# Kernel optimization log

Hardware: AMD Instinct MI355X
Metric: run time of the kernel (lower is better)

## Reference

```python
import jax, jax.numpy as jnp
import numpy as np

N_NODES = 100000
N_EDGES = 1600000
HIDDEN = 128
EF_DIM = 16
LAYERS = 2
N_GRAPHS = 64


def _residual(x, W, b):
    # Residual(mlp_num=2): x + act(act(x@W0+b0)@W1+b1), act = silu
    h = jax.nn.silu(x @ W[0] + b[0])
    h = jax.nn.silu(h @ W[1] + b[1])
    return x + h


def setup_inputs() -> dict:
    key = jax.random.key(0)
    ks = jax.random.split(key, 10)
    scalar = jax.random.normal(ks[0], (N_NODES, HIDDEN), jnp.float32)
    ef = jax.random.normal(ks[1], (N_EDGES, EF_DIM), jnp.float32)
    edge_index = jax.random.randint(ks[2], (2, N_EDGES), 0, N_NODES, jnp.int32)
    C = jax.random.uniform(ks[3], (N_NODES, 1), dtype=jnp.float32)
    conv_smooth = jax.random.uniform(ks[4], (N_EDGES, 1), dtype=jnp.float32)
    batch_index = jnp.sort(jax.random.randint(ks[5], (N_NODES,), 0, N_GRAPHS, jnp.int32))
    # per VD_Conv layer: emb0, emb1, conv0, conv1, out0, out1 residual blocks; + 3 pooling blocks
    n_res = LAYERS * 6 + 3
    res_W = jax.random.normal(ks[6], (n_res, 2, HIDDEN, HIDDEN), jnp.float32) * 0.02
    res_b = jnp.zeros((n_res, 2, HIDDEN), jnp.float32)
    e_lin = jax.random.normal(ks[7], (LAYERS, EF_DIM, HIDDEN), jnp.float32) * 0.02
    return {"scalar": scalar, "ef": ef, "edge_index": edge_index, "C": C,
            "conv_smooth": conv_smooth, "batch_index": batch_index,
            "res_W": res_W, "res_b": res_b, "e_lin": e_lin}


def reference(scalar, ef, edge_index, C, conv_smooth, batch_index, res_W, res_b, e_lin):
    row, col = edge_index[0], edge_index[1]
    for i in range(LAYERS):
        p = 6 * i
        s_src = _residual(scalar, res_W[p], res_b[p])
        s_dst = _residual(scalar, res_W[p + 1], res_b[p + 1])
        conv_filter = (ef @ e_lin[i]) * conv_smooth            # [E, H]
        scalar_edge = s_dst[col] * conv_filter                 # gather + elementwise filter
        conv = jax.ops.segment_sum(scalar_edge, row, num_segments=N_NODES) * C  # scatter-reduce (agg='sum')
        conv = _residual(_residual(conv, res_W[p + 2], res_b[p + 2]), res_W[p + 3], res_b[p + 3])
        s = s_src * conv
        s = _residual(_residual(s, res_W[p + 4], res_b[p + 4]), res_W[p + 5], res_b[p + 5])
        scalar = s + scalar                                    # outer residual in Vanilla_DisGNN
    graph = jax.ops.segment_sum(scalar, batch_index, num_segments=N_GRAPHS)
    q = 6 * LAYERS
    for j in range(3):
        graph = _residual(graph, res_W[q + j], res_b[q + j])
    return graph
```

## Files before the change

### kernel.cpp

```cpp
#include <hip/hip_runtime.h>
#include <hip/hip_bf16.h>
#include <cstdint>
#include <cstddef>

#define HD 128
#define WOFF 16384

typedef __bf16    bf16x8 __attribute__((ext_vector_type(8)));
typedef float     f32x4  __attribute__((ext_vector_type(4)));
typedef float     f32x16 __attribute__((ext_vector_type(16)));
typedef _Float16  h2     __attribute__((ext_vector_type(2)));
typedef _Float16  h8     __attribute__((ext_vector_type(8)));

typedef __attribute__((address_space(1))) const unsigned char ga_u8;
typedef __attribute__((address_space(3))) unsigned char lds_u8;

#if defined(__has_builtin)
#if __has_builtin(__builtin_amdgcn_fdot2)
#define HAVE_FDOT2 1
#endif
#endif

__device__ __forceinline__ float fdot2f(h2 a, h2 b, float c) {
#ifdef HAVE_FDOT2
    return __builtin_amdgcn_fdot2(a, b, c, false);
#else
    return c + (float)a[0]*(float)b[0] + (float)a[1]*(float)b[1];
#endif
}

__device__ __forceinline__ int swz(int r, int byteInRow) {
    int chunk = (byteInRow >> 4) ^ (r & 7);
    return r * 256 + (chunk << 4) + (byteInRow & 15);
}

__device__ __forceinline__ float silu_f(float v) { return v / (1.f + __expf(-v)); }

__device__ __forceinline__ int crow32(int r, int lane) {
    return (r & 3) + 8 * (r >> 2) + 4 * (lane >> 5);
}


__device__ __forceinline__ void issue_wstage(const __bf16* __restrict__ w, char* lds, int tid) {
    const int wv = tid >> 6, lane = tid & 63;
    const char* g = (const char*)w;
    #pragma unroll
    for (int i = 0; i < 4; ++i) {
        const int seg = (wv << 2) | i;
        __builtin_amdgcn_global_load_lds(
            (ga_u8*)(g + seg * 1024 + lane * 16),
            (lds_u8*)(lds + WOFF + seg * 1024),
            16, 0, 0);
    }
}

__device__ __forceinline__ void stage_x64(const float* __restrict__ x, char* lds,
                                          int r0, int nrows, int tid) {
    const int q = tid & 15;
    #pragma unroll
    for (int rr = 0; rr < 2; ++rr) {
        const int r  = (tid >> 4) + rr * 32;
        const int gr = r0 + r;
        float4 a = {0,0,0,0}, b = {0,0,0,0};
        if (gr < nrows) {
            const float4* p = (const float4*)(x + (size_t)gr * HD + q * 8);
            a = p[0]; b = p[1];
        }
        bf16x8 v;
        v[0]=(__bf16)a.x; v[1]=(__bf16)a.y; v[2]=(__bf16)a.z; v[3]=(__bf16)a.w;
        v[4]=(__bf16)b.x; v[5]=(__bf16)b.y; v[6]=(__bf16)b.z; v[7]=(__bf16)b.w;
        *(bf16x8*)(lds + swz(r, q * 16)) = v;
    }
}

__device__ __forceinline__ void mm_pass32(const char* lds, const float* __restrict__ bias,
                                          int rowtile, int coltile, int lane,
                                          f32x16& accA, f32x16& accB) {
    const int rowA = rowtile * 32 + (lane & 31);
    const int rowB = coltile * 32 + (lane & 31);
    const int kb   = (lane >> 5) * 16;
    bf16x8 afr[8];
    #pragma unroll
    for (int s = 0; s < 8; ++s)
        afr[s] = *(const bf16x8*)(lds + swz(rowA, s * 32 + kb));
    const float bv = bias[coltile * 32 + (lane & 31)];
    #pragma unroll
    for (int r = 0; r < 16; ++r) { accA[r] = bv; accB[r] = 0.f; }
    #pragma unroll
    for (int s = 0; s < 8; s += 2) {
        const bf16x8 b0 = *(const bf16x8*)(lds + WOFF + swz(rowB, s * 32 + kb));
        accA = __builtin_amdgcn_mfma_f32_32x32x16_bf16(afr[s], b0, accA, 0, 0, 0);
        const bf16x8 b1 = *(const bf16x8*)(lds + WOFF + swz(rowB, (s + 1) * 32 + kb));
        accB = __builtin_amdgcn_mfma_f32_32x32x16_bf16(afr[s + 1], b1, accB, 0, 0, 0);
    }
}

__device__ __forceinline__ void write_h32(char* lds, const f32x16& aA, const f32x16& aB,
                                          int rowtile, int coltile, int lane) {
    const int colb = (coltile * 32 + (lane & 31)) * 2;
    #pragma unroll
    for (int r = 0; r < 16; ++r)
        *(__bf16*)(lds + swz(rowtile * 32 + crow32(r, lane), colb)) =
            (__bf16)silu_f(aA[r] + aB[r]);
}

__device__ __forceinline__ void restage32(char* lds, const float carry[16],
                                          int rowtile, int coltile, int lane) {
    const int colb = (coltile * 32 + (lane & 31)) * 2;
    #pragma unroll
    for (int r = 0; r < 16; ++r)
        *(__bf16*)(lds + swz(rowtile * 32 + crow32(r, lane), colb)) = (__bf16)carry[r];
}

__global__ __launch_bounds__(512) void resid_dual_kernel(
    const float* __restrict__ x,
    const __bf16* __restrict__ wtA, const float* __restrict__ bA,
    const __bf16* __restrict__ wtB, const float* __restrict__ bB,
    __bf16* __restrict__ out1, __bf16* __restrict__ out2, int nrows)
{
    __shared__ char lds[49152];
    const int tid = threadIdx.x, lane = tid & 63, wv = tid >> 6;
    const int rowtile = wv >> 2, coltile = wv & 3;
    const int r0 = blockIdx.x * 64;
    const int colg = coltile * 32 + (lane & 31);

    issue_wstage(wtA, lds, tid);
    stage_x64(x, lds, r0, nrows, tid);
    f32x16 accA, accB;
    float xe[16];
    #pragma unroll
    for (int r = 0; r < 16; ++r) {
        const int gr = r0 + rowtile * 32 + crow32(r, lane);
        xe[r] = (gr < nrows) ? x[(size_t)gr * HD + colg] : 0.f;
    }
    __syncthreads();

    mm_pass32(lds, bA, rowtile, coltile, lane, accA, accB);
    __syncthreads();
    issue_wstage(wtA + 16384, lds, tid);
    write_h32(lds, accA, accB, rowtile, coltile, lane);
    __syncthreads();
    mm_pass32(lds, bA + HD, rowtile, coltile, lane, accA, accB);
    #pragma unroll
    for (int r = 0; r < 16; ++r) {
        const int gr = r0 + rowtile * 32 + crow32(r, lane);
        if (gr < nrows)
            out1[(size_t)gr * HD + colg] = (__bf16)(xe[r] + silu_f(accA[r] + accB[r]));
    }
    __syncthreads();
    issue_wstage(wtB, lds, tid);
    restage32(lds, xe, rowtile, coltile, lane);
    __syncthreads();
    mm_pass32(lds, bB, rowtile, coltile, lane, accA, accB);
    __syncthreads();
    issue_wstage(wtB + 16384, lds, tid);
    write_h32(lds, accA, accB, rowtile, coltile, lane);
    __syncthreads();
    mm_pass32(lds, bB + HD, rowtile, coltile, lane, accA, accB);
    #pragma unroll
    for (int r = 0; r < 16; ++r) {
        const int gr = r0 + rowtile * 32 + crow32(r, lane);
        if (gr < nrows)
            out2[(size_t)gr * HD + colg] = (__bf16)(xe[r] + silu_f(accA[r] + accB[r]));
    }
}

__global__ __launch_bounds__(512) void chain4_kernel(
    const float* __restrict__ x, const __bf16* __restrict__ mid,
    const __bf16* __restrict__ wA, const float* __restrict__ bA,
    const __bf16* __restrict__ wB, const float* __restrict__ bB,
    const __bf16* __restrict__ wC, const float* __restrict__ bC,
    const __bf16* __restrict__ wD, const float* __restrict__ bD,
    const float* __restrict__ post, float* __restrict__ y, int nrows)
{
    __shared__ char lds[49152];
    const int tid = threadIdx.x, lane = tid & 63, wv = tid >> 6;
    const int rowtile = wv >> 2, coltile = wv & 3;
    const int r0 = blockIdx.x * 64;
    const int colg = coltile * 32 + (lane & 31);

    issue_wstage(wA, lds, tid);
    stage_x64(x, lds, r0, nrows, tid);
    f32x16 accA, accB;
    float carry[16];
    #pragma unroll
    for (int r = 0; r < 16; ++r) {
        const int gr = r0 + rowtile * 32 + crow32(r, lane);
        carry[r] = (gr < nrows) ? x[(size_t)gr * HD + colg] : 0.f;
    }
    __syncthreads();

    mm_pass32(lds, bA, rowtile, coltile, lane, accA, accB);
    __syncthreads();
    issue_wstage(wA + 16384, lds, tid);
    write_h32(lds, accA, accB, rowtile, coltile, lane);
    __syncthreads();
    mm_pass32(lds, bA + HD, rowtile, coltile, lane, accA, accB);
    #pragma unroll
    for (int r = 0; r < 16; ++r) carry[r] += silu_f(accA[r] + accB[r]);
    __syncthreads();
    issue_wstage(wB, lds, tid);
    restage32(lds, carry, rowtile, coltile, lane);
    __syncthreads();
    mm_pass32(lds, bB, rowtile, coltile, lane, accA, accB);
    __syncthreads();
    issue_wstage(wB + 16384, lds, tid);
    write_h32(lds, accA, accB, rowtile, coltile, lane);
    __syncthreads();
    mm_pass32(lds, bB + HD, rowtile, coltile, lane, accA, accB);
    #pragma unroll
    for (int r = 0; r < 16; ++r) {
        const int gr = r0 + rowtile * 32 + crow32(r, lane);
        const float m = (gr < nrows) ? (float)mid[(size_t)gr * HD + colg] : 0.f;
        carry[r] = (carry[r] + silu_f(accA[r] + accB[r])) * m;
    }
    __syncthreads();
    issue_wstage(wC, lds, tid);
    restage32(lds, carry, rowtile, coltile, lane);
    __syncthreads();
    mm_pass32(lds, bC, rowtile, coltile, lane, accA, accB);
    __syncthreads();
    issue_wstage(wC + 16384, lds, tid);
    write_h32(lds, accA, accB, rowtile, coltile, lane);
    __syncthreads();
    mm_pass32(lds, bC + HD, rowtile, coltile, lane, accA, accB);
    #pragma unroll
    for (int r = 0; r < 16; ++r) carry[r] += silu_f(accA[r] + accB[r]);
    __syncthreads();
    issue_wstage(wD, lds, tid);
    restage32(lds, carry, rowtile, coltile, lane);
    __syncthreads();
    mm_pass32(lds, bD, rowtile, coltile, lane, accA, accB);
    __syncthreads();
    issue_wstage(wD + 16384, lds, tid);
    write_h32(lds, accA, accB, rowtile, coltile, lane);
    __syncthreads();
    mm_pass32(lds, bD + HD, rowtile, coltile, lane, accA, accB);
    #pragma unroll
    for (int r = 0; r < 16; ++r) {
        const int gr = r0 + rowtile * 32 + crow32(r, lane);
        if (gr < nrows)
            y[(size_t)gr * HD + colg] =
                carry[r] + silu_f(accA[r] + accB[r]) + post[(size_t)gr * HD + colg];
    }
}

__global__ __launch_bounds__(512) void chain3_kernel(
    const float* __restrict__ x,
    const __bf16* __restrict__ wA, const float* __restrict__ bA,
    const __bf16* __restrict__ wB, const float* __restrict__ bB,
    const __bf16* __restrict__ wC, const float* __restrict__ bC,
    float* __restrict__ y, int nrows)
{
    __shared__ char lds[49152];
    const int tid = threadIdx.x, lane = tid & 63, wv = tid >> 6;
    const int rowtile = wv >> 2, coltile = wv & 3;
    const int r0 = blockIdx.x * 64;
    const int colg = coltile * 32 + (lane & 31);

    issue_wstage(wA, lds, tid);
    stage_x64(x, lds, r0, nrows, tid);
    f32x16 accA, accB;
    float carry[16];
    #pragma unroll
    for (int r = 0; r < 16; ++r) {
        const int gr = r0 + rowtile * 32 + crow32(r, lane);
        carry[r] = (gr < nrows) ? x[(size_t)gr * HD + colg] : 0.f;
    }
    __syncthreads();

    const __bf16* w1s[3] = {wA + 16384, wB + 16384, wC + 16384};
    const __bf16* w0next[3] = {wB, wC, nullptr};
    const float* bs[3] = {bA, bB, bC};
    #pragma unroll
    for (int sb = 0; sb < 3; ++sb) {
        mm_pass32(lds, bs[sb], rowtile, coltile, lane, accA, accB);
        __syncthreads();
        issue_wstage(w1s[sb], lds, tid);
        write_h32(lds, accA, accB, rowtile, coltile, lane);
        __syncthreads();
        mm_pass32(lds, bs[sb] + HD, rowtile, coltile, lane, accA, accB);
        #pragma unroll
        for (int r = 0; r < 16; ++r) carry[r] += silu_f(accA[r] + accB[r]);
        if (sb < 2) {
            __syncthreads();
            issue_wstage(w0next[sb], lds, tid);
            restage32(lds, carry, rowtile, coltile, lane);
            __syncthreads();
        }
    }
    #pragma unroll
    for (int r = 0; r < 16; ++r) {
        const int gr = r0 + rowtile * 32 + crow32(r, lane);
        if (gr < nrows)
            y[(size_t)gr * HD + colg] = carry[r];
    }
}

__global__ __launch_bounds__(256) void hist_kernel(const int* __restrict__ erow, int* __restrict__ cnt, int E) {
    int i = blockIdx.x * blockDim.x + threadIdx.x;
    const int stride = gridDim.x * blockDim.x;
    for (; i < E; i += stride) atomicAdd(&cnt[erow[i]], 1);
}

__global__ __launch_bounds__(256) void scan1_kernel(const int* __restrict__ cnt, int* __restrict__ part, int n) {
    __shared__ int red[256];
    const int base = blockIdx.x * 1024;
    int s = 0;
    for (int i = threadIdx.x; i < 1024; i += 256) {
        const int idx = base + i;
        s += (idx < n) ? cnt[idx] : 0;
    }
    red[threadIdx.x] = s; __syncthreads();
    for (int o = 128; o > 0; o >>= 1) {
        if (threadIdx.x < o) red[threadIdx.x] += red[threadIdx.x + o];
        __syncthreads();
    }
    if (threadIdx.x == 0) part[blockIdx.x] = red[0];
}

__global__ __launch_bounds__(256) void scan2_kernel(int* __restrict__ part, int nb,
                                                    int* __restrict__ rowptr, int n) {
    __shared__ int sh[257];
    const int tid = threadIdx.x;
    int a[4]; int s = 0;
    #pragma unroll
    for (int q = 0; q < 4; ++q) {
        const int i = tid*4 + q;
        a[q] = (i < nb) ? part[i] : 0;
        s += a[q];
    }
    sh[tid + 1] = s; __syncthreads();
    if (tid == 0) {
        sh[0] = 0;
        int run = 0;
        for (int i = 1; i <= 256; ++i) { run += sh[i]; sh[i] = run; }
    }
    __syncthreads();
    int off = sh[tid];
    #pragma unroll
    for (int q = 0; q < 4; ++q) {
        const int i = tid*4 + q;
        if (i < nb) part[i] = off;
        off += a[q];
    }
    if (tid == 255) rowptr[n] = off;
}

__global__ __launch_bounds__(256) void scan3_kernel(const int* __restrict__ cnt, const int* __restrict__ part,
                                                    int* __restrict__ rowptr, int n) {
    __shared__ int sc[257];
    const int base = blockIdx.x * 1024;
    const int i0 = base + threadIdx.x * 4;
    int v[4]; int s = 0;
    #pragma unroll
    for (int q = 0; q < 4; ++q) {
        const int idx = i0 + q;
        v[q] = (idx < n) ? cnt[idx] : 0;
        s += v[q];
    }
    sc[threadIdx.x + 1] = s; __syncthreads();
    if (threadIdx.x == 0) {
        int run = 0;
        for (int i = 0; i < 256; ++i) { const int t = sc[i + 1]; sc[i + 1] = run; run += t; }
    }
    __syncthreads();
    int off = part[blockIdx.x] + sc[threadIdx.x + 1];
    #pragma unroll
    for (int q = 0; q < 4; ++q) {
        const int idx = i0 + q;
        if (idx < n) rowptr[idx] = off;
        off += v[q];
    }
}

__global__ __launch_bounds__(256) void scatter_reorder_kernel(
    const int* __restrict__ erow, const int* __restrict__ ecol,
    const float* __restrict__ ef, const float* __restrict__ cs,
    const int* __restrict__ rowptr, int* __restrict__ cursor,
    int* __restrict__ csr_col, _Float16* __restrict__ csr_ef, int E)
{
    int i = blockIdx.x * blockDim.x + threadIdx.x;
    const int stride = gridDim.x * blockDim.x;
    for (; i < E; i += stride) {
        const int r = erow[i];
        const int p = rowptr[r] + atomicAdd(&cursor[r], 1);
        csr_col[p] = ecol[i];
        const float c = cs[i];
        const float4* ep = (const float4*)(ef + (size_t)i * 16);
        const float4 e0 = ep[0], e1 = ep[1], e2 = ep[2], e3 = ep[3];
        h8 v0, v1;
        v0[0]=(_Float16)(e0.x*c); v0[1]=(_Float16)(e0.y*c); v0[2]=(_Float16)(e0.z*c); v0[3]=(_Float16)(e0.w*c);
        v0[4]=(_Float16)(e1.x*c); v0[5]=(_Float16)(e1.y*c); v0[6]=(_Float16)(e1.z*c); v0[7]=(_Float16)(e1.w*c);
        v1[0]=(_Float16)(e2.x*c); v1[1]=(_Float16)(e2.y*c); v1[2]=(_Float16)(e2.z*c); v1[3]=(_Float16)(e2.w*c);
        v1[4]=(_Float16)(e3.x*c); v1[5]=(_Float16)(e3.y*c); v1[6]=(_Float16)(e3.z*c); v1[7]=(_Float16)(e3.w*c);
        h8* dst = (h8*)(csr_ef + (size_t)p * 16);
        dst[0] = v0; dst[1] = v1;
    }
}

__global__ __launch_bounds__(256) void elin16_kernel(const float* __restrict__ elin,
                                                     _Float16* __restrict__ out, int total) {
    const int i = blockIdx.x * 256 + threadIdx.x;
    if (i < total) out[i] = (_Float16)elin[i];
}

__device__ __forceinline__ float bfu_lo(uint32_t u) { return __uint_as_float(u << 16); }
__device__ __forceinline__ float bfu_hi(uint32_t u) { return __uint_as_float(u & 0xffff0000u); }

__device__ __forceinline__ void edge_dot(const h8 a0, const h8 a1,
                                         const h2 w0[8], const h2 w1[8],
                                         float& f0, float& f1) {
    #pragma unroll
    for (int kk = 0; kk < 4; ++kk) {
        h2 p = {a0[2*kk], a0[2*kk+1]};
        f0 = fdot2f(p, w0[kk], f0);
        f1 = fdot2f(p, w1[kk], f1);
    }
    #pragma unroll
    for (int kk = 0; kk < 4; ++kk) {
        h2 p = {a1[2*kk], a1[2*kk+1]};
        f0 = fdot2f(p, w0[4+kk], f0);
        f1 = fdot2f(p, w1[4+kk], f1);
    }
}

__global__ __launch_bounds__(256) void conv_kernel(
    const _Float16* __restrict__ csr_ef, const int* __restrict__ csr_col,
    const _Float16* __restrict__ elin16, const int* __restrict__ rowptr,
    const __bf16* __restrict__ sdst, const float* __restrict__ Cn,
    float* __restrict__ conv, int nnodes)
{
    const int wv   = __builtin_amdgcn_readfirstlane(threadIdx.x >> 6);
    const int lane = threadIdx.x & 63;
    const int v = blockIdx.x * 4 + wv;
    if (v >= nnodes) return;
    const int j0 = lane * 2;

    h2 w0[8], w1[8];
    #pragma unroll
    for (int kk = 0; kk < 8; ++kk) {
        w0[kk][0] = elin16[(2*kk)   * HD + j0];
        w0[kk][1] = elin16[(2*kk+1) * HD + j0];
        w1[kk][0] = elin16[(2*kk)   * HD + j0 + 1];
        w1[kk][1] = elin16[(2*kk+1) * HD + j0 + 1];
    }

    const uint16_t* sd = (const uint16_t*)sdst;
    const int beg = rowptr[v], end = rowptr[v + 1];
    float acc0 = 0.f, acc1 = 0.f;
    int t = beg;
    for (; t + 8 <= end; t += 8) {
        int c[8];
        #pragma unroll
        for (int q = 0; q < 8; ++q) c[q] = csr_col[t + q];
        uint32_t u[8];
        #pragma unroll
        for (int q = 0; q < 8; ++q)
            u[q] = *(const uint32_t*)(sd + (size_t)c[q] * HD + j0);
        #pragma unroll
        for (int q = 0; q < 8; ++q) {
            const h8* ep = (const h8*)(csr_ef + (size_t)(t + q) * 16);
            const h8 a0 = ep[0], a1 = ep[1];
            float f0 = 0.f, f1 = 0.f;
            edge_dot(a0, a1, w0, w1, f0, f1);
            acc0 = fmaf(bfu_lo(u[q]), f0, acc0);
            acc1 = fmaf(bfu_hi(u[q]), f1, acc1);
        }
    }
    for (; t + 2 <= end; t += 2) {
        int c[2];
        c[0] = csr_col[t]; c[1] = csr_col[t + 1];
        uint32_t u[2];
        u[0] = *(const uint32_t*)(sd + (size_t)c[0] * HD + j0);
        u[1] = *(const uint32_t*)(sd + (size_t)c[1] * HD + j0);
        #pragma unroll
        for (int q = 0; q < 2; ++q) {
            const h8* ep = (const h8*)(csr_ef + (size_t)(t + q) * 16);
            const h8 a0 = ep[0], a1 = ep[1];
            float f0 = 0.f, f1 = 0.f;
            edge_dot(a0, a1, w0, w1, f0, f1);
            acc0 = fmaf(bfu_lo(u[q]), f0, acc0);
            acc1 = fmaf(bfu_hi(u[q]), f1, acc1);
        }
    }
    if (t < end) {
        const int c = csr_col[t];
        const uint32_t u = *(const uint32_t*)(sd + (size_t)c * HD + j0);
        const h8* ep = (const h8*)(csr_ef + (size_t)t * 16);
        const h8 a0 = ep[0], a1 = ep[1];
        float f0 = 0.f, f1 = 0.f;
        edge_dot(a0, a1, w0, w1, f0, f1);
        acc0 = fmaf(bfu_lo(u), f0, acc0);
        acc1 = fmaf(bfu_hi(u), f1, acc1);
    }
    const float cn = Cn[v];
    float2 out = {acc0 * cn, acc1 * cn};
    *(float2*)(conv + (size_t)v * HD + j0) = out;
}

__global__ __launch_bounds__(256) void pool_kernel(
    const float* __restrict__ s, const int* __restrict__ bidx,
    float* __restrict__ g, int n)
{
    const int slot = threadIdx.x >> 5;
    const int jc   = (threadIdx.x & 31) * 4;
    const int base = blockIdx.x * 256;
    if (base >= n) return;
    const int end = (base + 256 < n) ? base + 256 : n;
    float4 acc = {0,0,0,0};
    int cur = -1;
    for (int i = base + slot; i < end; i += 8) {
        const int b = bidx[i];
        if (b != cur) {
            if (cur >= 0) {
                atomicAdd(g + (size_t)cur*HD + jc + 0, acc.x);
                atomicAdd(g + (size_t)cur*HD + jc + 1, acc.y);
                atomicAdd(g + (size_t)cur*HD + jc + 2, acc.z);
                atomicAdd(g + (size_t)cur*HD + jc + 3, acc.w);
            }
            acc = {0,0,0,0};
            cur = b;
        }
        const float4 v = *(const float4*)(s + (size_t)i*HD + jc);
        acc.x += v.x; acc.y += v.y; acc.z += v.z; acc.w += v.w;
    }
    if (cur >= 0) {
        atomicAdd(g + (size_t)cur*HD + jc + 0, acc.x);
        atomicAdd(g + (size_t)cur*HD + jc + 1, acc.y);
        atomicAdd(g + (size_t)cur*HD + jc + 2, acc.z);
        atomicAdd(g + (size_t)cur*HD + jc + 3, acc.w);
    }
}

__global__ __launch_bounds__(256) void convw_kernel(const float* __restrict__ W, __bf16* __restrict__ wt, int total) {
    const int idx = blockIdx.x * 256 + threadIdx.x;
    if (idx >= total) return;
    const int mat = idx >> 14;
    const int rem = idx & 16383;
    const int j = rem >> 7;
    const int b = rem & 127;
    const int c = b >> 3, e = b & 7;
    const int k = ((c ^ (j & 7)) << 3) | e;
    wt[idx] = (__bf16)W[(size_t)mat * 16384 + k * HD + j];
}

extern "C" void kernel_launch(void* const* d_in, const int* in_sizes, int n_in,
                              void* d_out, int out_size, void* d_ws, size_t ws_size,
                              hipStream_t stream) {
    const float* scalar = (const float*)d_in[0];
    const float* ef     = (const float*)d_in[1];
    const int*   eidx   = (const int*)  d_in[2];
    const float* Cn     = (const float*)d_in[3];
    const float* cs     = (const float*)d_in[4];
    const int*   bidx   = (const int*)  d_in[5];
    const float* resW   = (const float*)d_in[6];
    const float* resB   = (const float*)d_in[7];
    const float* elin   = (const float*)d_in[8];

    const int N      = in_sizes[0] / HD;
    const int E      = in_sizes[1] / 16;
    const int n_res  = in_sizes[7] / (2 * HD);
    const int layers = (n_res - 3) / 6;
    const int G      = out_size / HD;
    const size_t nfeat = (size_t)N * HD;

    char* p = (char*)d_ws;
    auto alloc = [&](size_t bytes) { char* q = p; p += (bytes + 255) & ~(size_t)255; return q; };
    float*    A      = (float*)alloc(nfeat * 4);
    float*    Dc     = (float*)alloc(nfeat * 4);
    __bf16*   Bs16   = (__bf16*)alloc(nfeat * 2);
    __bf16*   Cs16   = (__bf16*)alloc(nfeat * 2);
    __bf16*   wt     = (__bf16*)alloc((size_t)n_res * 2 * 16384 * 2);
    float*    graph  = (float*)alloc((size_t)G * HD * 4);
    int*      rowptr = (int*)alloc((size_t)(N + 1) * 4);
    int*      rowcnt = (int*)alloc((size_t)N * 4);
    int*      csr_col= (int*)alloc((size_t)E * 4);
    _Float16* csr_ef = (_Float16*)alloc((size_t)E * 16 * 2);
    _Float16* elin16 = (_Float16*)alloc((size_t)layers * 16 * HD * 2);
    int*      part   = (int*)alloc(1024 * 4);

    const int* erow = eidx;
    const int* ecol = eidx + E;

    const int totW = n_res * 2 * 16384;
    convw_kernel<<<(totW + 255) / 256, 256, 0, stream>>>(resW, wt, totW);
    const int totE = layers * 16 * HD;
    elin16_kernel<<<(totE + 255) / 256, 256, 0, stream>>>(elin, elin16, totE);

    const int nchunks = (N + 1023) / 1024;
    hipMemsetAsync(rowcnt, 0, (size_t)N * 4, stream);
    hist_kernel<<<1024, 256, 0, stream>>>(erow, rowcnt, E);
    scan1_kernel<<<nchunks, 256, 0, stream>>>(rowcnt, part, N);
    scan2_kernel<<<1, 256, 0, stream>>>(part, nchunks, rowptr, N);
    scan3_kernel<<<nchunks, 256, 0, stream>>>(rowcnt, part, rowptr, N);
    hipMemsetAsync(rowcnt, 0, (size_t)N * 4, stream);
    scatter_reorder_kernel<<<1024, 256, 0, stream>>>(erow, ecol, ef, cs, rowptr, rowcnt, csr_col, csr_ef, E);

    const int gridR = (N + 63) / 64;
    const float* cur = scalar;
    for (int i = 0; i < layers; ++i) {
        const int pb = 6 * i;
        resid_dual_kernel<<<gridR, 512, 0, stream>>>(
            cur,
            wt + (size_t)pb * 32768, resB + (size_t)pb * 256,
            wt + (size_t)(pb + 1) * 32768, resB + (size_t)(pb + 1) * 256,
            Bs16, Cs16, N);
        conv_kernel<<<(N + 3) / 4, 256, 0, stream>>>(
            csr_ef, csr_col, elin16 + (size_t)i * 16 * HD, rowptr, Cs16, Cn, Dc, N);
        chain4_kernel<<<gridR, 512, 0, stream>>>(
            Dc, Bs16,
            wt + (size_t)(pb + 2) * 32768, resB + (size_t)(pb + 2) * 256,
            wt + (size_t)(pb + 3) * 32768, resB + (size_t)(pb + 3) * 256,
            wt + (size_t)(pb + 4) * 32768, resB + (size_t)(pb + 4) * 256,
            wt + (size_t)(pb + 5) * 32768, resB + (size_t)(pb + 5) * 256,
            cur, A, N);
        cur = A;
    }

    hipMemsetAsync(graph, 0, (size_t)G * HD * 4, stream);
    pool_kernel<<<(N + 255) / 256, 256, 0, stream>>>(cur, bidx, graph, N);

    const int q = 6 * layers;
    const int gridG = (G + 63) / 64;
    chain3_kernel<<<gridG, 512, 0, stream>>>(
        graph,
        wt + (size_t)q * 32768, resB + (size_t)q * 256,
        wt + (size_t)(q + 1) * 32768, resB + (size_t)(q + 1) * 256,
        wt + (size_t)(q + 2) * 32768, resB + (size_t)(q + 2) * 256,
        (float*)d_out, G);
}
```

Measured before the change: 876.0 us.

## Double-buffer weight staging in LDS and widen swizzle to 16 chunks

Adds a second LDS weight buffer to the fused residual-MLP kernels. The next weight matrix is now prefetched with global_load_lds while the current MFMA pass runs, instead of being loaded after a barrier, which hides weight-load latency behind compute. The LDS swizzle XOR pattern is widened from 8 to 16 chunks, matched in the weight pre-transform kernel, to cut bank conflicts. The cost is LDS use rising from 48KB to 80KB per block, which can lower the number of resident blocks per CU.

```diff
diff --git a/kernel.cpp b/kernel.cpp
--- a/kernel.cpp
+++ b/kernel.cpp
@@ -4,7 +4,9 @@
 #include <cstddef>
 
 #define HD 128
-#define WOFF 16384
+#define WB0 16384
+#define WB1 49152
+#define LDS_SZ 81920
 
 typedef __bf16    bf16x8 __attribute__((ext_vector_type(8)));
 typedef float     f32x4  __attribute__((ext_vector_type(4)));
@@ -30,7 +32,7 @@
 }
 
 __device__ __forceinline__ int swz(int r, int byteInRow) {
-    int chunk = (byteInRow >> 4) ^ (r & 7);
+    int chunk = (byteInRow >> 4) ^ (r & 15);
     return r * 256 + (chunk << 4) + (byteInRow & 15);
 }
 
@@ -41,7 +43,8 @@
 }
 
 
-__device__ __forceinline__ void issue_wstage(const __bf16* __restrict__ w, char* lds, int tid) {
+__device__ __forceinline__ void issue_wstage(const __bf16* __restrict__ w, char* lds,
+                                             int woff, int tid) {
     const int wv = tid >> 6, lane = tid & 63;
     const char* g = (const char*)w;
     #pragma unroll
@@ -49,7 +52,7 @@
         const int seg = (wv << 2) | i;
         __builtin_amdgcn_global_load_lds(
             (ga_u8*)(g + seg * 1024 + lane * 16),
-            (lds_u8*)(lds + WOFF + seg * 1024),
+            (lds_u8*)(lds + woff + seg * 1024),
             16, 0, 0);
     }
 }
@@ -73,7 +76,8 @@
     }
 }
 
-__device__ __forceinline__ void mm_pass32(const char* lds, const float* __restrict__ bias,
+__device__ __forceinline__ void mm_pass32(const char* lds, int woff,
+                                          const float* __restrict__ bias,
                                           int rowtile, int coltile, int lane,
                                           f32x16& accA, f32x16& accB) {
     const int rowA = rowtile * 32 + (lane & 31);
@@ -88,9 +92,9 @@
     for (int r = 0; r < 16; ++r) { accA[r] = bv; accB[r] = 0.f; }
     #pragma unroll
     for (int s = 0; s < 8; s += 2) {
-        const bf16x8 b0 = *(const bf16x8*)(lds + WOFF + swz(rowB, s * 32 + kb));
+        const bf16x8 b0 = *(const bf16x8*)(lds + woff + swz(rowB, s * 32 + kb));
         accA = __builtin_amdgcn_mfma_f32_32x32x16_bf16(afr[s], b0, accA, 0, 0, 0);
-        const bf16x8 b1 = *(const bf16x8*)(lds + WOFF + swz(rowB, (s + 1) * 32 + kb));
+        const bf16x8 b1 = *(const bf16x8*)(lds + woff + swz(rowB, (s + 1) * 32 + kb));
         accB = __builtin_amdgcn_mfma_f32_32x32x16_bf16(afr[s + 1], b1, accB, 0, 0, 0);
     }
 }
@@ -118,13 +122,13 @@
     const __bf16* __restrict__ wtB, const float* __restrict__ bB,
     __bf16* __restrict__ out1, __bf16* __restrict__ out2, int nrows)
 {
-    __shared__ char lds[49152];
+    __shared__ char lds[LDS_SZ];
     const int tid = threadIdx.x, lane = tid & 63, wv = tid >> 6;
     const int rowtile = wv >> 2, coltile = wv & 3;
     const int r0 = blockIdx.x * 64;
     const int colg = coltile * 32 + (lane & 31);
 
-    issue_wstage(wtA, lds, tid);
+    issue_wstage(wtA, lds, WB0, tid);
     stage_x64(x, lds, r0, nrows, tid);
     f32x16 accA, accB;
     float xe[16];
@@ -135,12 +139,13 @@
     }
     __syncthreads();
 
-    mm_pass32(lds, bA, rowtile, coltile, lane, accA, accB);
-    __syncthreads();
-    issue_wstage(wtA + 16384, lds, tid);
-    write_h32(lds, accA, accB, rowtile, coltile, lane);
-    __syncthreads();
-    mm_pass32(lds, bA + HD, rowtile, coltile, lane, accA, accB);
+    issue_wstage(wtA + 16384, lds, WB1, tid);
+    mm_pass32(lds, WB0, bA, rowtile, coltile, lane, accA, accB);
+    __syncthreads();
+    write_h32(lds, accA, accB, rowtile, coltile, lane);
+    __syncthreads();
+    issue_wstage(wtB, lds, WB0, tid);
+    mm_pass32(lds, WB1, bA + HD, rowtile, coltile, lane, accA, accB);
     #pragma unroll
     for (int r = 0; r < 16; ++r) {
         const int gr = r0 + rowtile * 32 + crow32(r, lane);
@@ -148,15 +153,14 @@
             out1[(size_t)gr * HD + colg] = (__bf16)(xe[r] + silu_f(accA[r] + accB[r]));
     }
     __syncthreads();
-    issue_wstage(wtB, lds, tid);
     restage32(lds, xe, rowtile, coltile, lane);
     __syncthreads();
-    mm_pass32(lds, bB, rowtile, coltile, lane, accA, accB);
-    __syncthreads();
-    issue_wstage(wtB + 16384, lds, tid);
-    write_h32(lds, accA, accB, rowtile, coltile, lane);
-    __syncthreads();
-    mm_pass32(lds, bB + HD, rowtile, coltile, lane, accA, accB);
+    issue_wstage(wtB + 16384, lds, WB1, tid);
+    mm_pass32(lds, WB0, bB, rowtile, coltile, lane, accA, accB);
+    __syncthreads();
+    write_h32(lds, accA, accB, rowtile, coltile, lane);
+    __syncthreads();
+    mm_pass32(lds, WB1, bB + HD, rowtile, coltile, lane, accA, accB);
     #pragma unroll
     for (int r = 0; r < 16; ++r) {
         const int gr = r0 + rowtile * 32 + crow32(r, lane);
@@ -173,13 +177,13 @@
     const __bf16* __restrict__ wD, const float* __restrict__ bD,
     const float* __restrict__ post, float* __restrict__ y, int nrows)
 {
-    __shared__ char lds[49152];
+    __shared__ char lds[LDS_SZ];
     const int tid = threadIdx.x, lane = tid & 63, wv = tid >> 6;
     const int rowtile = wv >> 2, coltile = wv & 3;
     const int r0 = blockIdx.x * 64;
     const int colg = coltile * 32 + (lane & 31);
 
-    issue_wstage(wA, lds, tid);
+    issue_wstage(wA, lds, WB0, tid);
     stage_x64(x, lds, r0, nrows, tid);
     f32x16 accA, accB;
     float carry[16];
@@ -190,24 +194,25 @@
     }
     __syncthreads();
 
-    mm_pass32(lds, bA, rowtile, coltile, lane, accA, accB);
-    __syncthreads();
-    issue_wstage(wA + 16384, lds, tid);
-    write_h32(lds, accA, accB, rowtile, coltile, lane);
-    __syncthreads();
-    mm_pass32(lds, bA + HD, rowtile, coltile, lane, accA, accB);
+    issue_wstage(wA + 16384, lds, WB1, tid);
+    mm_pass32(lds, WB0, bA, rowtile, coltile, lane, accA, accB);
+    __syncthreads();
+    write_h32(lds, accA, accB, rowtile, coltile, lane);
+    __syncthreads();
+    issue_wstage(wB, lds, WB0, tid);
+    mm_pass32(lds, WB1, bA + HD, rowtile, coltile, lane, accA, accB);
     #pragma unroll
     for (int r = 0; r < 16; ++r) carry[r] += silu_f(accA[r] + accB[r]);
     __syncthreads();
-    issue_wstage(wB, lds, tid);
     restage32(lds, carry, rowtile, coltile, lane);
     __syncthreads();
-    mm_pass32(lds, bB, rowtile, coltile, lane, accA, accB);
-    __syncthreads();
-    issue_wstage(wB + 16384, lds, tid);
-    write_h32(lds, accA, accB, rowtile, coltile, lane);
-    __syncthreads();
-    mm_pass32(lds, bB + HD, rowtile, coltile, lane, accA, accB);
+    issue_wstage(wB + 16384, lds, WB1, tid);
+    mm_pass32(lds, WB0, bB, rowtile, coltile, lane, accA, accB);
+    __syncthreads();
+    write_h32(lds, accA, accB, rowtile, coltile, lane);
+    __syncthreads();
+    issue_wstage(wC, lds, WB0, tid);
+    mm_pass32(lds, WB1, bB + HD, rowtile, coltile, lane, accA, accB);
     #pragma unroll
     for (int r = 0; r < 16; ++r) {
         const int gr = r0 + rowtile * 32 + crow32(r, lane);
@@ -215,27 +220,26 @@
         carry[r] = (carry[r] + silu_f(accA[r] + accB[r])) * m;
     }
     __syncthreads();
-    issue_wstage(wC, lds, tid);
     restage32(lds, carry, rowtile, coltile, lane);
     __syncthreads();
-    mm_pass32(lds, bC, rowtile, coltile, lane, accA, accB);
-    __syncthreads();
-    issue_wstage(wC + 16384, lds, tid);
-    write_h32(lds, accA, accB, rowtile, coltile, lane);
-    __syncthreads();
-    mm_pass32(lds, bC + HD, rowtile, coltile, lane, accA, accB);
+    issue_wstage(wC + 16384, lds, WB1, tid);
+    mm_pass32(lds, WB0, bC, rowtile, coltile, lane, accA, accB);
+    __syncthreads();
+    write_h32(lds, accA, accB, rowtile, coltile, lane);
+    __syncthreads();
+    issue_wstage(wD, lds, WB0, tid);
+    mm_pass32(lds, WB1, bC + HD, rowtile, coltile, lane, accA, accB);
     #pragma unroll
     for (int r = 0; r < 16; ++r) carry[r] += silu_f(accA[r] + accB[r]);
     __syncthreads();
-    issue_wstage(wD, lds, tid);
     restage32(lds, carry, rowtile, coltile, lane);
     __syncthreads();
-    mm_pass32(lds, bD, rowtile, coltile, lane, accA, accB);
-    __syncthreads();
-    issue_wstage(wD + 16384, lds, tid);
-    write_h32(lds, accA, accB, rowtile, coltile, lane);
-    __syncthreads();
-    mm_pass32(lds, bD + HD, rowtile, coltile, lane, accA, accB);
+    issue_wstage(wD + 16384, lds, WB1, tid);
+    mm_pass32(lds, WB0, bD, rowtile, coltile, lane, accA, accB);
+    __syncthreads();
+    write_h32(lds, accA, accB, rowtile, coltile, lane);
+    __syncthreads();
+    mm_pass32(lds, WB1, bD + HD, rowtile, coltile, lane, accA, accB);
     #pragma unroll
     for (int r = 0; r < 16; ++r) {
         const int gr = r0 + rowtile * 32 + crow32(r, lane);
@@ -252,13 +256,13 @@
     const __bf16* __restrict__ wC, const float* __restrict__ bC,
     float* __restrict__ y, int nrows)
 {
-    __shared__ char lds[49152];
+    __shared__ char lds[LDS_SZ];
     const int tid = threadIdx.x, lane = tid & 63, wv = tid >> 6;
     const int rowtile = wv >> 2, coltile = wv & 3;
     const int r0 = blockIdx.x * 64;
     const int colg = coltile * 32 + (lane & 31);
 
-    issue_wstage(wA, lds, tid);
+    issue_wstage(wA, lds, WB0, tid);
     stage_x64(x, lds, r0, nrows, tid);
     f32x16 accA, accB;
     float carry[16];
@@ -269,31 +273,41 @@
     }
     __syncthreads();
 
-    const __bf16* w1s[3] = {wA + 16384, wB + 16384, wC + 16384};
-    const __bf16* w0next[3] = {wB, wC, nullptr};
-    const float* bs[3] = {bA, bB, bC};
-    #pragma unroll
-    for (int sb = 0; sb < 3; ++sb) {
-        mm_pass32(lds, bs[sb], rowtile, coltile, lane, accA, accB);
-        __syncthreads();
-        issue_wstage(w1s[sb], lds, tid);
-        write_h32(lds, accA, accB, rowtile, coltile, lane);
-        __syncthreads();
-        mm_pass32(lds, bs[sb] + HD, rowtile, coltile, lane, accA, accB);
-        #pragma unroll
-        for (int r = 0; r < 16; ++r) carry[r] += silu_f(accA[r] + accB[r]);
-        if (sb < 2) {
-            __syncthreads();
-            issue_wstage(w0next[sb], lds, tid);
-            restage32(lds, carry, rowtile, coltile, lane);
-            __syncthreads();
-        }
-    }
+    issue_wstage(wA + 16384, lds, WB1, tid);
+    mm_pass32(lds, WB0, bA, rowtile, coltile, lane, accA, accB);
+    __syncthreads();
+    write_h32(lds, accA, accB, rowtile, coltile, lane);
+    __syncthreads();
+    issue_wstage(wB, lds, WB0, tid);
+    mm_pass32(lds, WB1, bA + HD, rowtile, coltile, lane, accA, accB);
+    #pragma unroll
+    for (int r = 0; r < 16; ++r) carry[r] += silu_f(accA[r] + accB[r]);
+    __syncthreads();
+    restage32(lds, carry, rowtile, coltile, lane);
+    __syncthreads();
+    issue_wstage(wB + 16384, lds, WB1, tid);
+    mm_pass32(lds, WB0, bB, rowtile, coltile, lane, accA, accB);
+    __syncthreads();
+    write_h32(lds, accA, accB, rowtile, coltile, lane);
+    __syncthreads();
+    issue_wstage(wC, lds, WB0, tid);
+    mm_pass32(lds, WB1, bB + HD, rowtile, coltile, lane, accA, accB);
+    #pragma unroll
+    for (int r = 0; r < 16; ++r) carry[r] += silu_f(accA[r] + accB[r]);
+    __syncthreads();
+    restage32(lds, carry, rowtile, coltile, lane);
+    __syncthreads();
+    issue_wstage(wC + 16384, lds, WB1, tid);
+    mm_pass32(lds, WB0, bC, rowtile, coltile, lane, accA, accB);
+    __syncthreads();
+    write_h32(lds, accA, accB, rowtile, coltile, lane);
+    __syncthreads();
+    mm_pass32(lds, WB1, bC + HD, rowtile, coltile, lane, accA, accB);
     #pragma unroll
     for (int r = 0; r < 16; ++r) {
         const int gr = r0 + rowtile * 32 + crow32(r, lane);
         if (gr < nrows)
-            y[(size_t)gr * HD + colg] = carry[r];
+            y[(size_t)gr * HD + colg] = carry[r] + silu_f(accA[r] + accB[r]);
     }
 }
 
@@ -541,7 +555,7 @@
     const int j = rem >> 7;
     const int b = rem & 127;
     const int c = b >> 3, e = b & 7;
-    const int k = ((c ^ (j & 7)) << 3) | e;
+    const int k = ((c ^ (j & 15)) << 3) | e;
     wt[idx] = (__bf16)W[(size_t)mat * 16384 + k * HD + j];
 }
 
```

Result: slower. 913.1 us (+4.2%).

## Load MFMA weight fragments directly from global memory and double-buffer activations in LDS

Applied to the files above, without the earlier changes.

The MLP kernels no longer stage weight matrices into LDS. The weights are pre-permuted into an MFMA fragment layout, so each wave loads its B fragments straight from global memory, which are likely cache-resident. Activations now ping-pong between two LDS regions, which removes about half of the __syncthreads barriers and cuts LDS to 32KB with launch bounds asking for 4 blocks per CU. The change also widens the swizzle to 16 chunks and uses a fast reciprocal in silu. The risk is extra global and L2 traffic for weights in every block, plus register pressure from holding 8 weight fragments per wave.

```diff
diff --git a/kernel.cpp b/kernel.cpp
--- a/kernel.cpp
+++ b/kernel.cpp
@@ -4,7 +4,9 @@
 #include <cstddef>
 
 #define HD 128
-#define WOFF 16384
+#define R0OFF 0
+#define R1OFF 16384
+#define DATA_LDS 32768
 
 typedef __bf16    bf16x8 __attribute__((ext_vector_type(8)));
 typedef float     f32x4  __attribute__((ext_vector_type(4)));
@@ -12,12 +14,12 @@
 typedef _Float16  h2     __attribute__((ext_vector_type(2)));
 typedef _Float16  h8     __attribute__((ext_vector_type(8)));
 
-typedef __attribute__((address_space(1))) const unsigned char ga_u8;
-typedef __attribute__((address_space(3))) unsigned char lds_u8;
-
 #if defined(__has_builtin)
 #if __has_builtin(__builtin_amdgcn_fdot2)
 #define HAVE_FDOT2 1
+#endif
+#if __has_builtin(__builtin_amdgcn_rcpf)
+#define HAVE_RCPF 1
 #endif
 #endif
 
@@ -29,38 +31,31 @@
 #endif
 }
 
+__device__ __forceinline__ float silu_f(float v) {
+#ifdef HAVE_RCPF
+    return v * __builtin_amdgcn_rcpf(1.f + __expf(-v));
+#else
+    return v / (1.f + __expf(-v));
+#endif
+}
+
 __device__ __forceinline__ int swz(int r, int byteInRow) {
-    int chunk = (byteInRow >> 4) ^ (r & 7);
+    int chunk = (byteInRow >> 4) ^ (r & 15);
     return r * 256 + (chunk << 4) + (byteInRow & 15);
 }
-
-__device__ __forceinline__ float silu_f(float v) { return v / (1.f + __expf(-v)); }
 
 __device__ __forceinline__ int crow32(int r, int lane) {
     return (r & 3) + 8 * (r >> 2) + 4 * (lane >> 5);
-}
-
-
-__device__ __forceinline__ void issue_wstage(const __bf16* __restrict__ w, char* lds, int tid) {
-    const int wv = tid >> 6, lane = tid & 63;
-    const char* g = (const char*)w;
-    #pragma unroll
-    for (int i = 0; i < 4; ++i) {
-        const int seg = (wv << 2) | i;
-        __builtin_amdgcn_global_load_lds(
-            (ga_u8*)(g + seg * 1024 + lane * 16),
-            (lds_u8*)(lds + WOFF + seg * 1024),
-            16, 0, 0);
-    }
 }
 
 __device__ __forceinline__ void stage_x64(const float* __restrict__ x, char* lds,
                                           int r0, int nrows, int tid) {
     const int q = tid & 15;
+    const int r  = tid >> 4;
     #pragma unroll
     for (int rr = 0; rr < 2; ++rr) {
-        const int r  = (tid >> 4) + rr * 32;
-        const int gr = r0 + r;
+        const int row = r + rr * 32;
+        const int gr = r0 + row;
         float4 a = {0,0,0,0}, b = {0,0,0,0};
         if (gr < nrows) {
             const float4* p = (const float4*)(x + (size_t)gr * HD + q * 8);
@@ -69,103 +64,97 @@
         bf16x8 v;
         v[0]=(__bf16)a.x; v[1]=(__bf16)a.y; v[2]=(__bf16)a.z; v[3]=(__bf16)a.w;
         v[4]=(__bf16)b.x; v[5]=(__bf16)b.y; v[6]=(__bf16)b.z; v[7]=(__bf16)b.w;
-        *(bf16x8*)(lds + swz(r, q * 16)) = v;
-    }
-}
-
-__device__ __forceinline__ void mm_pass32(const char* lds, const float* __restrict__ bias,
-                                          int rowtile, int coltile, int lane,
+        *(bf16x8*)(lds + swz(row, q * 16)) = v;
+    }
+}
+
+__device__ __forceinline__ void mm_pass_g(const char* lds, int roff,
+                                          const __bf16* __restrict__ wf,
+                                          const float* __restrict__ bias,
+                                          int rt, int ct, int lane,
                                           f32x16& accA, f32x16& accB) {
-    const int rowA = rowtile * 32 + (lane & 31);
-    const int rowB = coltile * 32 + (lane & 31);
+    const int rowA = rt * 32 + (lane & 31);
     const int kb   = (lane >> 5) * 16;
-    bf16x8 afr[8];
+    const __bf16* wbase = wf + ct * 4096 + lane * 8;
+    bf16x8 wfr[8];
     #pragma unroll
     for (int s = 0; s < 8; ++s)
-        afr[s] = *(const bf16x8*)(lds + swz(rowA, s * 32 + kb));
-    const float bv = bias[coltile * 32 + (lane & 31)];
+        wfr[s] = *(const bf16x8*)(wbase + s * 512);
+    const float bv = bias[ct * 32 + (lane & 31)];
     #pragma unroll
     for (int r = 0; r < 16; ++r) { accA[r] = bv; accB[r] = 0.f; }
     #pragma unroll
     for (int s = 0; s < 8; s += 2) {
-        const bf16x8 b0 = *(const bf16x8*)(lds + WOFF + swz(rowB, s * 32 + kb));
-        accA = __builtin_amdgcn_mfma_f32_32x32x16_bf16(afr[s], b0, accA, 0, 0, 0);
-        const bf16x8 b1 = *(const bf16x8*)(lds + WOFF + swz(rowB, (s + 1) * 32 + kb));
-        accB = __builtin_amdgcn_mfma_f32_32x32x16_bf16(afr[s + 1], b1, accB, 0, 0, 0);
-    }
-}
-
-__device__ __forceinline__ void write_h32(char* lds, const f32x16& aA, const f32x16& aB,
-                                          int rowtile, int coltile, int lane) {
-    const int colb = (coltile * 32 + (lane & 31)) * 2;
+        const bf16x8 a0 = *(const bf16x8*)(lds + roff + swz(rowA, s * 32 + kb));
+        accA = __builtin_amdgcn_mfma_f32_32x32x16_bf16(a0, wfr[s], accA, 0, 0, 0);
+        const bf16x8 a1 = *(const bf16x8*)(lds + roff + swz(rowA, (s + 1) * 32 + kb));
+        accB = __builtin_amdgcn_mfma_f32_32x32x16_bf16(a1, wfr[s + 1], accB, 0, 0, 0);
+    }
+}
+
+__device__ __forceinline__ void write_h32(char* lds, int roff, const f32x16& aA, const f32x16& aB,
+                                          int rt, int ct, int lane) {
+    const int colb = (ct * 32 + (lane & 31)) * 2;
     #pragma unroll
     for (int r = 0; r < 16; ++r)
-        *(__bf16*)(lds + swz(rowtile * 32 + crow32(r, lane), colb)) =
+        *(__bf16*)(lds + roff + swz(rt * 32 + crow32(r, lane), colb)) =
             (__bf16)silu_f(aA[r] + aB[r]);
 }
 
-__device__ __forceinline__ void restage32(char* lds, const float carry[16],
-                                          int rowtile, int coltile, int lane) {
-    const int colb = (coltile * 32 + (lane & 31)) * 2;
+__device__ __forceinline__ void restage32(char* lds, int roff, const float carry[16],
+                                          int rt, int ct, int lane) {
+    const int colb = (ct * 32 + (lane & 31)) * 2;
     #pragma unroll
     for (int r = 0; r < 16; ++r)
-        *(__bf16*)(lds + swz(rowtile * 32 + crow32(r, lane), colb)) = (__bf16)carry[r];
-}
-
-__global__ __launch_bounds__(512) void resid_dual_kernel(
+        *(__bf16*)(lds + roff + swz(rt * 32 + crow32(r, lane), colb)) = (__bf16)carry[r];
+}
+
+__global__ __launch_bounds__(512, 4) void resid_dual_kernel(
     const float* __restrict__ x,
     const __bf16* __restrict__ wtA, const float* __restrict__ bA,
     const __bf16* __restrict__ wtB, const float* __restrict__ bB,
     __bf16* __restrict__ out1, __bf16* __restrict__ out2, int nrows)
 {
-    __shared__ char lds[49152];
+    __shared__ char lds[DATA_LDS];
     const int tid = threadIdx.x, lane = tid & 63, wv = tid >> 6;
-    const int rowtile = wv >> 2, coltile = wv & 3;
+    const int rt = wv >> 2, ct = wv & 3;
     const int r0 = blockIdx.x * 64;
-    const int colg = coltile * 32 + (lane & 31);
-
-    issue_wstage(wtA, lds, tid);
+    const int colg = ct * 32 + (lane & 31);
+
     stage_x64(x, lds, r0, nrows, tid);
     f32x16 accA, accB;
     float xe[16];
     #pragma unroll
     for (int r = 0; r < 16; ++r) {
-        const int gr = r0 + rowtile * 32 + crow32(r, lane);
+        const int gr = r0 + rt * 32 + crow32(r, lane);
         xe[r] = (gr < nrows) ? x[(size_t)gr * HD + colg] : 0.f;
     }
     __syncthreads();
 
-    mm_pass32(lds, bA, rowtile, coltile, lane, accA, accB);
-    __syncthreads();
-    issue_wstage(wtA + 16384, lds, tid);
-    write_h32(lds, accA, accB, rowtile, coltile, lane);
-    __syncthreads();
-    mm_pass32(lds, bA + HD, rowtile, coltile, lane, accA, accB);
-    #pragma unroll
-    for (int r = 0; r < 16; ++r) {
-        const int gr = r0 + rowtile * 32 + crow32(r, lane);
+    mm_pass_g(lds, R0OFF, wtA, bA, rt, ct, lane, accA, accB);
+    write_h32(lds, R1OFF, accA, accB, rt, ct, lane);
+    __syncthreads();
+    mm_pass_g(lds, R1OFF, wtA + 16384, bA + HD, rt, ct, lane, accA, accB);
+    #pragma unroll
+    for (int r = 0; r < 16; ++r) {
+        const int gr = r0 + rt * 32 + crow32(r, lane);
         if (gr < nrows)
             out1[(size_t)gr * HD + colg] = (__bf16)(xe[r] + silu_f(accA[r] + accB[r]));
     }
     __syncthreads();
-    issue_wstage(wtB, lds, tid);
-    restage32(lds, xe, rowtile, coltile, lane);
-    __syncthreads();
-    mm_pass32(lds, bB, rowtile, coltile, lane, accA, accB);
-    __syncthreads();
-    issue_wstage(wtB + 16384, lds, tid);
-    write_h32(lds, accA, accB, rowtile, coltile, lane);
-    __syncthreads();
-    mm_pass32(lds, bB + HD, rowtile, coltile, lane, accA, accB);
-    #pragma unroll
-    for (int r = 0; r < 16; ++r) {
-        const int gr = r0 + rowtile * 32 + crow32(r, lane);
+    mm_pass_g(lds, R0OFF, wtB, bB, rt, ct, lane, accA, accB);
+    write_h32(lds, R1OFF, accA, accB, rt, ct, lane);
+    __syncthreads();
+    mm_pass_g(lds, R1OFF, wtB + 16384, bB + HD, rt, ct, lane, accA, accB);
+    #pragma unroll
+    for (int r = 0; r < 16; ++r) {
+        const int gr = r0 + rt * 32 + crow32(r, lane);
         if (gr < nrows)
             out2[(size_t)gr * HD + colg] = (__bf16)(xe[r] + silu_f(accA[r] + accB[r]));
     }
 }
 
-__global__ __launch_bounds__(512) void chain4_kernel(
+__global__ __launch_bounds__(512, 4) void chain4_kernel(
     const float* __restrict__ x, const __bf16* __restrict__ mid,
     const __bf16* __restrict__ wA, const float* __restrict__ bA,
     const __bf16* __restrict__ wB, const float* __restrict__ bB,
@@ -173,127 +162,111 @@
     const __bf16* __restrict__ wD, const float* __restrict__ bD,
     const float* __restrict__ post, float* __restrict__ y, int nrows)
 {
-    __shared__ char lds[49152];
+    __shared__ char lds[DATA_LDS];
     const int tid = threadIdx.x, lane = tid & 63, wv = tid >> 6;
-    const int rowtile = wv >> 2, coltile = wv & 3;
+    const int rt = wv >> 2, ct = wv & 3;
     const int r0 = blockIdx.x * 64;
-    const int colg = coltile * 32 + (lane & 31);
-
-    issue_wstage(wA, lds, tid);
+    const int colg = ct * 32 + (lane & 31);
+
     stage_x64(x, lds, r0, nrows, tid);
     f32x16 accA, accB;
     float carry[16];
     #pragma unroll
     for (int r = 0; r < 16; ++r) {
-        const int gr = r0 + rowtile * 32 + crow32(r, lane);
+        const int gr = r0 + rt * 32 + crow32(r, lane);
         carry[r] = (gr < nrows) ? x[(size_t)gr * HD + colg] : 0.f;
     }
     __syncthreads();
 
-    mm_pass32(lds, bA, rowtile, coltile, lane, accA, accB);
-    __syncthreads();
-    issue_wstage(wA + 16384, lds, tid);
-    write_h32(lds, accA, accB, rowtile, coltile, lane);
-    __syncthreads();
-    mm_pass32(lds, bA + HD, rowtile, coltile, lane, accA, accB);
+    mm_pass_g(lds, R0OFF, wA, bA, rt, ct, lane, accA, accB);
+    write_h32(lds, R1OFF, accA, accB, rt, ct, lane);
+    __syncthreads();
+    mm_pass_g(lds, R1OFF, wA + 16384, bA + HD, rt, ct, lane, accA, accB);
     #pragma unroll
     for (int r = 0; r < 16; ++r) carry[r] += silu_f(accA[r] + accB[r]);
-    __syncthreads();
-    issue_wstage(wB, lds, tid);
-    restage32(lds, carry, rowtile, coltile, lane);
-    __syncthreads();
-    mm_pass32(lds, bB, rowtile, coltile, lane, accA, accB);
-    __syncthreads();
-    issue_wstage(wB + 16384, lds, tid);
-    write_h32(lds, accA, accB, rowtile, coltile, lane);
-    __syncthreads();
-    mm_pass32(lds, bB + HD, rowtile, coltile, lane, accA, accB);
-    #pragma unroll
-    for (int r = 0; r < 16; ++r) {
-        const int gr = r0 + rowtile * 32 + crow32(r, lane);
+    restage32(lds, R0OFF, carry, rt, ct, lane);
+    __syncthreads();
+    mm_pass_g(lds, R0OFF, wB, bB, rt, ct, lane, accA, accB);
+    write_h32(lds, R1OFF, accA, accB, rt, ct, lane);
+    __syncthreads();
+    mm_pass_g(lds, R1OFF, wB + 16384, bB + HD, rt, ct, lane, accA, accB);
+    #pragma unroll
+    for (int r = 0; r < 16; ++r) {
+        const int gr = r0 + rt * 32 + crow32(r, lane);
         const float m = (gr < nrows) ? (float)mid[(size_t)gr * HD + colg] : 0.f;
         carry[r] = (carry[r] + silu_f(accA[r] + accB[r])) * m;
     }
-    __syncthreads();
-    issue_wstage(wC, lds, tid);
-    restage32(lds, carry, rowtile, coltile, lane);
-    __syncthreads();
-    mm_pass32(lds, bC, rowtile, coltile, lane, accA, accB);
-    __syncthreads();
-    issue_wstage(wC + 16384, lds, tid);
-    write_h32(lds, accA, accB, rowtile, coltile, lane);
-    __syncthreads();
-    mm_pass32(lds, bC + HD, rowtile, coltile, lane, accA, accB);
+    restage32(lds, R0OFF, carry, rt, ct, lane);
+    __syncthreads();
+    mm_pass_g(lds, R0OFF, wC, bC, rt, ct, lane, accA, accB);
+    write_h32(lds, R1OFF, accA, accB, rt, ct, lane);
+    __syncthreads();
+    mm_pass_g(lds, R1OFF, wC + 16384, bC + HD, rt, ct, lane, accA, accB);
     #pragma unroll
     for (int r = 0; r < 16; ++r) carry[r] += silu_f(accA[r] + accB[r]);
-    __syncthreads();
-    issue_wstage(wD, lds, tid);
-    restage32(lds, carry, rowtile, coltile, lane);
-    __syncthreads();
-    mm_pass32(lds, bD, rowtile, coltile, lane, accA, accB);
-    __syncthreads();
-    issue_wstage(wD + 16384, lds, tid);
-    write_h32(lds, accA, accB, rowtile, coltile, lane);
-    __syncthreads();
-    mm_pass32(lds, bD + HD, rowtile, coltile, lane, accA, accB);
-    #pragma unroll
-    for (int r = 0; r < 16; ++r) {
-        const int gr = r0 + rowtile * 32 + crow32(r, lane);
+    restage32(lds, R0OFF, carry, rt, ct, lane);
+    __syncthreads();
+    mm_pass_g(lds, R0OFF, wD, bD, rt, ct, lane, accA, accB);
+    write_h32(lds, R1OFF, accA, accB, rt, ct, lane);
+    __syncthreads();
+    mm_pass_g(lds, R1OFF, wD + 16384, bD + HD, rt, ct, lane, accA, accB);
+    #pragma unroll
+    for (int r = 0; r < 16; ++r) {
+        const int gr = r0 + rt * 32 + crow32(r, lane);
         if (gr < nrows)
             y[(size_t)gr * HD + colg] =
                 carry[r] + silu_f(accA[r] + accB[r]) + post[(size_t)gr * HD + colg];
     }
 }
 
-__global__ __launch_bounds__(512) void chain3_kernel(
+__global__ __launch_bounds__(512, 4) void chain3_kernel(
     const float* __restrict__ x,
     const __bf16* __restrict__ wA, const float* __restrict__ bA,
     const __bf16* __restrict__ wB, const float* __restrict__ bB,
     const __bf16* __restrict__ wC, const float* __restrict__ bC,
     float* __restrict__ y, int nrows)
 {
-    __shared__ char lds[49152];
+    __shared__ char lds[DATA_LDS];
     const int tid = threadIdx.x, lane = tid & 63, wv = tid >> 6;
-    const int rowtile = wv >> 2, coltile = wv & 3;
+    const int rt = wv >> 2, ct = wv & 3;
     const int r0 = blockIdx.x * 64;
-    const int colg = coltile * 32 + (lane & 31);
-
-    issue_wstage(wA, lds, tid);
+    const int colg = ct * 32 + (lane & 31);
+
     stage_x64(x, lds, r0, nrows, tid);
     f32x16 accA, accB;
     float carry[16];
     #pragma unroll
     for (int r = 0; r < 16; ++r) {
-        const int gr = r0 + rowtile * 32 + crow32(r, lane);
+        const int gr = r0 + rt * 32 + crow32(r, lane);
         carry[r] = (gr < nrows) ? x[(size_t)gr * HD + colg] : 0.f;
     }
     __syncthreads();
 
-    const __bf16* w1s[3] = {wA + 16384, wB + 16384, wC + 16384};
-    const __bf16* w0next[3] = {wB, wC, nullptr};
-    const float* bs[3] = {bA, bB, bC};
-    #pragma unroll
-    for (int sb = 0; sb < 3; ++sb) {
-        mm_pass32(lds, bs[sb], rowtile, coltile, lane, accA, accB);
-        __syncthreads();
-        issue_wstage(w1s[sb], lds, tid);
-        write_h32(lds, accA, accB, rowtile, coltile, lane);
-        __syncthreads();
-        mm_pass32(lds, bs[sb] + HD, rowtile, coltile, lane, accA, accB);
-        #pragma unroll
-        for (int r = 0; r < 16; ++r) carry[r] += silu_f(accA[r] + accB[r]);
-        if (sb < 2) {
-            __syncthreads();
-            issue_wstage(w0next[sb], lds, tid);
-            restage32(lds, carry, rowtile, coltile, lane);
-            __syncthreads();
-        }
-    }
-    #pragma unroll
-    for (int r = 0; r < 16; ++r) {
-        const int gr = r0 + rowtile * 32 + crow32(r, lane);
+    mm_pass_g(lds, R0OFF, wA, bA, rt, ct, lane, accA, accB);
+    write_h32(lds, R1OFF, accA, accB, rt, ct, lane);
+    __syncthreads();
+    mm_pass_g(lds, R1OFF, wA + 16384, bA + HD, rt, ct, lane, accA, accB);
+    #pragma unroll
+    for (int r = 0; r < 16; ++r) carry[r] += silu_f(accA[r] + accB[r]);
+    restage32(lds, R0OFF, carry, rt, ct, lane);
+    __syncthreads();
+    mm_pass_g(lds, R0OFF, wB, bB, rt, ct, lane, accA, accB);
+    write_h32(lds, R1OFF, accA, accB, rt, ct, lane);
+    __syncthreads();
+    mm_pass_g(lds, R1OFF, wB + 16384, bB + HD, rt, ct, lane, accA, accB);
+    #pragma unroll
+    for (int r = 0; r < 16; ++r) carry[r] += silu_f(accA[r] + accB[r]);
+    restage32(lds, R0OFF, carry, rt, ct, lane);
+    __syncthreads();
+    mm_pass_g(lds, R0OFF, wC, bC, rt, ct, lane, accA, accB);
+    write_h32(lds, R1OFF, accA, accB, rt, ct, lane);
+    __syncthreads();
+    mm_pass_g(lds, R1OFF, wC + 16384, bC + HD, rt, ct, lane, accA, accB);
+    #pragma unroll
+    for (int r = 0; r < 16; ++r) {
+        const int gr = r0 + rt * 32 + crow32(r, lane);
         if (gr < nrows)
-            y[(size_t)gr * HD + colg] = carry[r];
+            y[(size_t)gr * HD + colg] = carry[r] + silu_f(accA[r] + accB[r]);
     }
 }
 
@@ -536,12 +509,13 @@
 __global__ __launch_bounds__(256) void convw_kernel(const float* __restrict__ W, __bf16* __restrict__ wt, int total) {
     const int idx = blockIdx.x * 256 + threadIdx.x;
     if (idx >= total) return;
-    const int mat = idx >> 14;
-    const int rem = idx & 16383;
-    const int j = rem >> 7;
-    const int b = rem & 127;
-    const int c = b >> 3, e = b & 7;
-    const int k = ((c ^ (j & 7)) << 3) | e;
+    const int mat  = idx >> 14;
+    const int e    = idx & 7;
+    const int lane = (idx >> 3) & 63;
+    const int s    = (idx >> 9) & 7;
+    const int ct   = (idx >> 12) & 3;
+    const int j = ct * 32 + (lane & 31);
+    const int k = s * 16 + ((lane >> 5) << 3) + e;
     wt[idx] = (__bf16)W[(size_t)mat * 16384 + k * HD + j];
 }
 
```

Result: faster. 749.8 us (-14.4%).
